# Performance work log

Hardware: AMD Instinct MI355X
Metric: run time of the kernel (lower is better)

The kernel has to match this reference:

```python
import jax, jax.numpy as jnp
import numpy as np

K_NEIGHBORS = 50
MEM_WEIGHT = 0.9  # min(0.9, write_count/10000) saturated
LN_EPS = 1e-5
DIST_EPS = 1e-7


def setup_inputs() -> dict:
    key = jax.random.key(0)
    ks = jax.random.split(key, 10)
    B, S, H, D, M = 4096, 544, 256, 128, 50000
    sc = lambda fan: 1.0 / np.sqrt(fan)
    return {
        "states": jax.random.normal(ks[0], (B, S), jnp.float32),
        "W1": jax.random.normal(ks[1], (S, H), jnp.float32) * sc(S),
        "b1": jnp.zeros((H,), jnp.float32),
        "W2": jax.random.normal(ks[2], (H, D), jnp.float32) * sc(H),
        "b2": jnp.zeros((D,), jnp.float32),
        "ln_g": jnp.ones((D,), jnp.float32),
        "ln_b": jnp.zeros((D,), jnp.float32),
        "mem_keys": jax.random.normal(ks[3], (M, D), jnp.float32),
        "mem_values": jax.random.normal(ks[4], (M,), jnp.float32),
        "V1": jax.random.normal(ks[5], (S, H), jnp.float32) * sc(S),
        "c1": jnp.zeros((H,), jnp.float32),
        "V2": jax.random.normal(ks[6], (H, D), jnp.float32) * sc(H),
        "c2": jnp.zeros((D,), jnp.float32),
        "V3": jax.random.normal(ks[7], (D, 1), jnp.float32) * sc(D),
        "c3": jnp.zeros((1,), jnp.float32),
    }


def _layernorm(x, g, b):
    mu = jnp.mean(x, axis=-1, keepdims=True)
    var = jnp.var(x, axis=-1, keepdims=True)
    return (x - mu) * jax.lax.rsqrt(var + LN_EPS) * g + b


def reference(states, W1, b1, W2, b2, ln_g, ln_b, mem_keys, mem_values,
              V1, c1, V2, c2, V3, c3):
    # --- key encoder: Linear -> ReLU -> Linear -> LayerNorm ---
    h = jax.nn.relu(states @ W1 + b1)            # [B, 256]
    q = _layernorm(h @ W2 + b2, ln_g, ln_b)      # [B, 128]

    # --- DND lookup: squared L2 kNN (FAISS IndexFlatL2 semantics) ---
    # dist2[b, m] = ||q_b - k_m||^2
    q2 = jnp.sum(q * q, axis=-1, keepdims=True)          # [B, 1]
    k2 = jnp.sum(mem_keys * mem_keys, axis=-1)           # [M]
    dist2 = q2 + k2[None, :] - 2.0 * (q @ mem_keys.T)    # [B, M]
    neg_top, idx = jax.lax.top_k(-dist2, K_NEIGHBORS)    # [B, k]
    d = -neg_top                                         # smallest k distances
    w = 1.0 / (d + DIST_EPS)
    w = w / jnp.sum(w, axis=-1, keepdims=True)
    mem_val = jnp.sum(w * mem_values[idx], axis=-1)      # [B]

    # --- value network ---
    v = jax.nn.relu(states @ V1 + c1)
    v = jax.nn.relu(v @ V2 + c2)
    net_val = (v @ V3 + c3)[:, 0]                        # [B]

    return MEM_WEIGHT * mem_val + (1.0 - MEM_WEIGHT) * net_val
```

## Files before the change

kernel.cpp:

```cpp
#include <hip/hip_runtime.h>
#include <stdint.h>

#define B_   4096
#define S_   544
#define H_   256
#define D_   128
#define M_   50000
#define KNN  50
#define NSLICE 8
#define SL_REAL 6250
#define BKEY 64
#define NB   98
#define SL_PAD (NB * BKEY)
#define CAP  128
#define RR   64
#define IMG_U32 5120
#define QT   8

typedef unsigned long long u64;
typedef unsigned int u32;
typedef __attribute__((ext_vector_type(8))) __bf16 bf16x8;
typedef __attribute__((ext_vector_type(8))) unsigned short u16x8;
typedef __attribute__((ext_vector_type(4))) float f32x4;
typedef __attribute__((ext_vector_type(4))) u32 u32x4;

__device__ __forceinline__ u32 bf16_rne(float x) {
  u32 u = __float_as_uint(x);
  return (u + 0x7FFFu + ((u >> 16) & 1u)) >> 16;
}

__device__ __forceinline__ void gl_lds16(const u32* g, u32* l) {
  __builtin_amdgcn_global_load_lds(
      (const __attribute__((address_space(1))) u32*)g,
      (__attribute__((address_space(3))) u32*)l, 16, 0, 0);
}

__global__ __launch_bounds__(256) void k1_gemm(
    const float* __restrict__ A,
    const float* __restrict__ W1, const float* __restrict__ b1,
    const float* __restrict__ V1, const float* __restrict__ c1,
    float* __restrict__ hout, float* __restrict__ v1out)
{
  const float* W    = (blockIdx.z == 0) ? W1 : V1;
  const float* bias = (blockIdx.z == 0) ? b1 : c1;
  float* out        = (blockIdx.z == 0) ? hout : v1out;

  __shared__ float as[16][68];
  __shared__ float bs[16][64];

  int tid = threadIdx.x;
  int tx = tid & 15, ty = tid >> 4;
  int rb = blockIdx.y * 64, cb = blockIdx.x * 64;

  float acc[4][4] = {};

  for (int k0 = 0; k0 < S_; k0 += 16) {
    {
      int r = tid >> 2, k4 = (tid & 3) << 2;
      float4 a = *(const float4*)&A[(size_t)(rb + r) * S_ + k0 + k4];
      as[k4 + 0][r] = a.x; as[k4 + 1][r] = a.y;
      as[k4 + 2][r] = a.z; as[k4 + 3][r] = a.w;
    }
    {
      int kk = tid >> 4, c4 = (tid & 15) << 2;
      *(float4*)&bs[kk][c4] = *(const float4*)&W[(size_t)(k0 + kk) * H_ + cb + c4];
    }
    __syncthreads();
#pragma unroll
    for (int kk = 0; kk < 16; ++kk) {
      float4 a4 = *(const float4*)&as[kk][ty << 2];
      float4 b4 = *(const float4*)&bs[kk][tx << 2];
      float av[4] = {a4.x, a4.y, a4.z, a4.w};
      float bv[4] = {b4.x, b4.y, b4.z, b4.w};
#pragma unroll
      for (int i = 0; i < 4; ++i)
#pragma unroll
        for (int j = 0; j < 4; ++j)
          acc[i][j] = fmaf(av[i], bv[j], acc[i][j]);
    }
    __syncthreads();
  }

#pragma unroll
  for (int i = 0; i < 4; ++i) {
    int r = rb + (ty << 2) + i;
#pragma unroll
    for (int j = 0; j < 4; ++j) {
      int c = cb + (tx << 2) + j;
      float v = acc[i][j] + bias[c];
      out[(size_t)r * H_ + c] = v > 0.0f ? v : 0.0f;
    }
  }
}

__global__ __launch_bounds__(256) void k2_fused(
    const float* __restrict__ A0,
    const float* __restrict__ A1,
    const float* __restrict__ W2, const float* __restrict__ b2,
    const float* __restrict__ V2, const float* __restrict__ c2,
    const float* __restrict__ lng, const float* __restrict__ lnb,
    const float* __restrict__ V3, const float* __restrict__ c3,
    ushort* __restrict__ qext2, float* __restrict__ qrow,
    float* __restrict__ q2out, float* __restrict__ netout)
{
  __shared__ float as[32][36];
  __shared__ float bs[32][132];
  __shared__ float yt[32][132];
  __shared__ float v3s[128];

  int mode = blockIdx.z;
  const float* A    = mode ? A1 : A0;
  const float* W    = mode ? V2 : W2;
  const float* bias = mode ? c2 : b2;

  int tid = threadIdx.x;
  int tx = tid & 31, ty = tid >> 5;
  int rb = blockIdx.x * 32;

  if (mode == 1 && tid < 128) v3s[tid] = V3[tid];

  float acc[4][4] = {};

  for (int k0 = 0; k0 < H_; k0 += 32) {
    {
      int r = tid >> 3, k4 = (tid & 7) << 2;
      float4 a = *(const float4*)&A[(size_t)(rb + r) * H_ + k0 + k4];
      as[k4 + 0][r] = a.x; as[k4 + 1][r] = a.y;
      as[k4 + 2][r] = a.z; as[k4 + 3][r] = a.w;
    }
    {
      int kk = tid >> 3, c16 = (tid & 7) << 4;
#pragma unroll
      for (int t = 0; t < 4; ++t)
        *(float4*)&bs[kk][c16 + (t << 2)] =
            *(const float4*)&W[(size_t)(k0 + kk) * D_ + c16 + (t << 2)];
    }
    __syncthreads();
#pragma unroll
    for (int kk = 0; kk < 32; ++kk) {
      float4 a4 = *(const float4*)&as[kk][ty << 2];
      float4 b4 = *(const float4*)&bs[kk][tx << 2];
      float av[4] = {a4.x, a4.y, a4.z, a4.w};
      float bv[4] = {b4.x, b4.y, b4.z, b4.w};
#pragma unroll
      for (int i = 0; i < 4; ++i)
#pragma unroll
        for (int j = 0; j < 4; ++j)
          acc[i][j] = fmaf(av[i], bv[j], acc[i][j]);
    }
    __syncthreads();
  }

#pragma unroll
  for (int i = 0; i < 4; ++i)
#pragma unroll
    for (int j = 0; j < 4; ++j) {
      int c = (tx << 2) + j;
      yt[(ty << 2) + i][c] = acc[i][j] + bias[c];
    }
  __syncthreads();

  int r8 = tid >> 3, j8 = tid & 7;
  int rg = rb + r8;
  if (mode == 0) {
    float s = 0.f;
#pragma unroll
    for (int t = 0; t < 16; ++t) s += yt[r8][(j8 << 4) + t];
    s += __shfl_xor(s, 1); s += __shfl_xor(s, 2); s += __shfl_xor(s, 4);
    float mu = s * (1.0f / 128.0f);
    float vs = 0.f;
#pragma unroll
    for (int t = 0; t < 16; ++t) {
      float d = yt[r8][(j8 << 4) + t] - mu;
      vs = fmaf(d, d, vs);
    }
    vs += __shfl_xor(vs, 1); vs += __shfl_xor(vs, 2); vs += __shfl_xor(vs, 4);
    float var = vs * (1.0f / 128.0f);
    float rstd = 1.0f / sqrtf(var + 1e-5f);
    float q2p = 0.f;
    ushort* qe = qext2 + (size_t)rg * 128;
#pragma unroll
    for (int t = 0; t < 16; ++t) {
      int c = (j8 << 4) + t;
      float qv = (yt[r8][c] - mu) * rstd * lng[c] + lnb[c];
      qrow[(size_t)rg * D_ + c] = qv;
      qe[c] = (ushort)bf16_rne(-2.0f * qv);
      q2p = fmaf(qv, qv, q2p);
    }
    q2p += __shfl_xor(q2p, 1); q2p += __shfl_xor(q2p, 2); q2p += __shfl_xor(q2p, 4);
    if (j8 == 0) q2out[rg] = q2p;
  } else {
    float s = 0.f;
#pragma unroll
    for (int t = 0; t < 16; ++t) {
      int c = (j8 << 4) + t;
      float v = yt[r8][c];
      v = v > 0.f ? v : 0.f;
      s = fmaf(v, v3s[c], s);
    }
    s += __shfl_xor(s, 1); s += __shfl_xor(s, 2); s += __shfl_xor(s, 4);
    if (j8 == 0) netout[rg] = s + c3[0];
  }
}

__global__ __launch_bounds__(256) void k5_keyimg(
    const float* __restrict__ keys, u32* __restrict__ keyimg,
    float* __restrict__ k2out)
{
  int tid = threadIdx.x;
  int p = blockIdx.x * 128 + (tid >> 1);
  int sub = tid & 1;
  int slice = p / SL_PAD;
  int within = p - slice * SL_PAD;
  int kb = within >> 6, kib = within & 63;
  u32* img = keyimg + (size_t)(slice * NB + kb) * IMG_U32;
  bool real = within < SL_REAL;

  u32 w[32];
  float ss = 0.f;
  if (real) {
    const float* kp = keys + (size_t)(slice * SL_REAL + within) * D_ + sub * 64;
#pragma unroll
    for (int i = 0; i < 16; ++i) {
      float4 x = *(const float4*)(kp + i * 4);
      ss = fmaf(x.x, x.x, fmaf(x.y, x.y, fmaf(x.z, x.z, fmaf(x.w, x.w, ss))));
      w[i * 2]     = bf16_rne(x.x) | (bf16_rne(x.y) << 16);
      w[i * 2 + 1] = bf16_rne(x.z) | (bf16_rne(x.w) << 16);
    }
  } else {
#pragma unroll
    for (int i = 0; i < 32; ++i) w[i] = 0;
  }
#pragma unroll
  for (int cc = 0; cc < 2; ++cc) {
    int c = sub * 2 + cc;
#pragma unroll
    for (int j = 0; j < 4; ++j) {
      u32x4 v = {w[cc*16 + j*4], w[cc*16 + j*4 + 1], w[cc*16 + j*4 + 2], w[cc*16 + j*4 + 3]};
      *(u32x4*)&img[c * 1024 + j * 256 + kib * 4] = v;
    }
  }
  float tot = ss + __shfl_xor(ss, 1);
  if (sub == 0) {
    u32 w0;
    if (real) {
      k2out[slice * SL_REAL + within] = tot;
      u32 h = bf16_rne(tot);
      float hf = __uint_as_float(h << 16);
      u32 lo = bf16_rne(tot - hf);
      w0 = h | (lo << 16);
    } else {
      w0 = 0x7FC07FC0u;
    }
    u32x4 v0 = {w0, 0, 0, 0};
    u32x4 z  = {0, 0, 0, 0};
    *(u32x4*)&img[4 * 1024 + 0 * 256 + kib * 4] = v0;
    *(u32x4*)&img[4 * 1024 + 1 * 256 + kib * 4] = z;
    *(u32x4*)&img[4 * 1024 + 2 * 256 + kib * 4] = z;
    *(u32x4*)&img[4 * 1024 + 3 * 256 + kib * 4] = z;
  }
}

__device__ __forceinline__ void sort128_wave(u32* sb, int lane) {
  for (int k = 2; k <= 128; k <<= 1)
    for (int j = k >> 1; j > 0; j >>= 1) {
#pragma unroll
      for (int half = 0; half < 2; ++half) {
        int e = lane + (half << 6);
        int pp = e ^ j;
        if (pp > e) {
          u32 x = sb[e], y = sb[pp];
          bool up = ((e & k) == 0);
          if ((x > y) == up) { sb[e] = y; sb[pp] = x; }
        }
      }
      __builtin_amdgcn_wave_barrier();
    }
}

#define CSWAP(A, B) do { u32 lo_ = (A) < (B) ? (A) : (B);           \
    u32 hi_ = (A) < (B) ? (B) : (A); (A) = lo_; (B) = hi_; } while (0)

__global__ __launch_bounds__(1024, 8) void k3_knn(
    const ushort* __restrict__ qext2,
    const float* __restrict__ q2g,
    const u32* __restrict__ keyimg,
    u32* __restrict__ lbuf)
{
  __shared__ u32 kbuf[2][IMG_U32];

  int tid = threadIdx.x;
  int l = tid & 63, w = tid >> 6;
  int l15 = l & 15, l4 = l >> 4;
  int wr = w & 3, wc = w >> 2;
  int slice = blockIdx.x & 7;
  int rb = (blockIdx.x >> 3) << 6;

  bf16x8 bfr[4];
#pragma unroll
  for (int c = 0; c < 4; ++c) {
    const ushort* qp = qext2 + (size_t)(rb + wc * 16 + l15) * 128 + c * 32 + l4 * 8;
    bfr[c] = __builtin_bit_cast(bf16x8, *(const u32x4*)qp);
  }
  bf16x8 bk2;
  {
    u16x8 v = {0, 0, 0, 0, 0, 0, 0, 0};
    if (l4 == 0) { v[0] = 0x3F80; v[1] = 0x3F80; }
    bk2 = __builtin_bit_cast(bf16x8, v);
  }
  float q2v = q2g[rb + wc * 16 + l15];

  u32 topq[QT];
#pragma unroll
  for (int j = 0; j < QT; ++j) topq[j] = 0xFFFFFFFFu;

  const u32* imgbase = keyimg + (size_t)slice * NB * IMG_U32;

  auto stage = [&](int b, int t) {
    if (w < 5) {
      const u32* src = imgbase + (size_t)t * IMG_U32 + w * 1024 + l * 4;
      u32* dst = &kbuf[b][w * 1024];
#pragma unroll
      for (int i = 0; i < 4; ++i)
        gl_lds16(src + i * 256, dst + i * 256);
    }
  };

  stage(0, 0);
  __syncthreads();

  int cur = 0;
  for (int t = 0; t < NB; ++t) {
    if (t + 1 < NB) stage(cur ^ 1, t + 1);

    f32x4 acc = {};
#pragma unroll
    for (int c = 0; c < 5; ++c) {
      bf16x8 a = __builtin_bit_cast(bf16x8,
          *(const u32x4*)&kbuf[cur][c * 1024 + l4 * 256 + (wr * 16 + l15) * 4]);
      acc = __builtin_amdgcn_mfma_f32_16x16x32_bf16(a, (c < 4) ? bfr[c] : bk2, acc, 0, 0, 0);
    }

    u32 cc[4];
#pragma unroll
    for (int r = 0; r < 4; ++r) {
      float dd = q2v + acc[r];
      cc[r] = (__float_as_uint(dd) & 0xFFFFE000u) |
              (u32)(t * BKEY + wr * 16 + (l4 << 2) + r);
    }
    CSWAP(cc[0], cc[1]); CSWAP(cc[2], cc[3]);
    CSWAP(cc[0], cc[2]); CSWAP(cc[1], cc[3]);
    CSWAP(cc[1], cc[2]);
    topq[7] = topq[7] < cc[0] ? topq[7] : cc[0];
    topq[6] = topq[6] < cc[1] ? topq[6] : cc[1];
    topq[5] = topq[5] < cc[2] ? topq[5] : cc[2];
    topq[4] = topq[4] < cc[3] ? topq[4] : cc[3];
    CSWAP(topq[0], topq[4]); CSWAP(topq[1], topq[5]);
    CSWAP(topq[2], topq[6]); CSWAP(topq[3], topq[7]);
    CSWAP(topq[0], topq[2]); CSWAP(topq[1], topq[3]);
    CSWAP(topq[4], topq[6]); CSWAP(topq[5], topq[7]);
    CSWAP(topq[0], topq[1]); CSWAP(topq[2], topq[3]);
    CSWAP(topq[4], topq[5]); CSWAP(topq[6], topq[7]);

    __syncthreads();
    cur ^= 1;
  }

  __syncthreads();
  u32* mb = &kbuf[0][0];

#pragma unroll 1
  for (int g = 0; g < 4; ++g) {
    if (wc == g) {
      u32* dst = mb + l15 * 128 + (wr * 4 + l4) * QT;
#pragma unroll
      for (int j = 0; j < QT; ++j) dst[j] = topq[j];
    }
    __syncthreads();

    sort128_wave(mb + w * 128, l);

    if (l < KNN) {
      int grow = rb + g * 16 + w;
      lbuf[((size_t)grow * NSLICE + slice) * CAP + l] = mb[w * 128 + l];
    }
    __syncthreads();
  }
}

__global__ __launch_bounds__(256) void k4_rerank(
    const u32* __restrict__ lbuf, const float* __restrict__ qrow,
    const float* __restrict__ q2g, const float* __restrict__ k2g,
    const float* __restrict__ keys, const float* __restrict__ memv,
    const float* __restrict__ net, float* __restrict__ out)
{
  __shared__ u64 sb[512];
  __shared__ float qs[128];
  __shared__ float part[4][RR];
  __shared__ u64 cand[RR];
  int b = blockIdx.x, t = threadIdx.x;
  if (t < 128) qs[t] = qrow[(size_t)b * D_ + t];
#pragma unroll
  for (int h = 0; h < 2; ++h) {
    int e = t + (h << 8);
    u64 v = ~0ull;
    if (e < NSLICE * KNN) {
      int s = e / KNN, j = e - s * KNN;
      u32 k32 = lbuf[((size_t)b * NSLICE + s) * CAP + j];
      v = ((u64)(k32 & 0xFFFFE000u) << 32) | (u32)(s * SL_REAL + (k32 & 0x1FFFu));
    }
    sb[e] = v;
  }
  __syncthreads();
  for (int k = 2; k <= 512; k <<= 1)
    for (int j = k >> 1; j > 0; j >>= 1) {
#pragma unroll
      for (int h = 0; h < 2; ++h) {
        int e = t + (h << 8);
        int p = e ^ j;
        if (p > e) {
          u64 x = sb[e], y = sb[p];
          bool up = ((e & k) == 0);
          if ((x > y) == up) { sb[e] = y; sb[p] = x; }
        }
      }
      __syncthreads();
    }

  int cid = t & 63, g = t >> 6;
  u32 gidx = (u32)sb[cid];
  const float* kp = keys + (size_t)gidx * D_ + g * 32;
  float dot = 0.f;
#pragma unroll
  for (int i = 0; i < 8; ++i) {
    float4 kv = *(const float4*)(kp + i * 4);
    float4 qv = *(const float4*)&qs[g * 32 + i * 4];
    dot = fmaf(kv.x, qv.x, dot); dot = fmaf(kv.y, qv.y, dot);
    dot = fmaf(kv.z, qv.z, dot); dot = fmaf(kv.w, qv.w, dot);
  }
  part[g][cid] = dot;
  __syncthreads();
  if (t < RR) {
    float dotf = part[0][t] + part[1][t] + part[2][t] + part[3][t];
    u32 gi = (u32)sb[t];
    float dd = q2g[b] + k2g[gi] - 2.0f * dotf;
    cand[t] = ((u64)__float_as_uint(dd) << 32) | gi;
  }
  __syncthreads();
  if (t < 64) {
    for (int k = 2; k <= 64; k <<= 1)
      for (int j = k >> 1; j > 0; j >>= 1) {
        u64 x = cand[t], y = cand[t ^ j];
        __builtin_amdgcn_wave_barrier();
        bool up = ((t & k) == 0);
        u64 mn = x < y ? x : y, mx = x < y ? y : x;
        cand[t] = ((t < (t ^ j)) == up) ? mn : mx;
        __builtin_amdgcn_wave_barrier();
      }
    u64 key = cand[t];
    float d = __uint_as_float((u32)(key >> 32));
    u32 idx = (u32)key;
    float w = 0.f, wv = 0.f;
    if (t < KNN) {
      float ww = 1.0f / (d + 1e-7f);
      w = ww;
      wv = ww * memv[idx];
    }
#pragma unroll
    for (int o = 1; o < 64; o <<= 1) {
      w += __shfl_xor(w, o);
      wv += __shfl_xor(wv, o);
    }
    if (t == 0) out[b] = 0.9f * (wv / w) + 0.1f * net[b];
  }
}

extern "C" void kernel_launch(void* const* d_in, const int* in_sizes, int n_in,
                              void* d_out, int out_size, void* d_ws, size_t ws_size,
                              hipStream_t stream)
{
  const float* states     = (const float*)d_in[0];
  const float* W1         = (const float*)d_in[1];
  const float* b1         = (const float*)d_in[2];
  const float* W2         = (const float*)d_in[3];
  const float* b2         = (const float*)d_in[4];
  const float* lng        = (const float*)d_in[5];
  const float* lnb        = (const float*)d_in[6];
  const float* mem_keys   = (const float*)d_in[7];
  const float* mem_values = (const float*)d_in[8];
  const float* V1         = (const float*)d_in[9];
  const float* c1         = (const float*)d_in[10];
  const float* V2         = (const float*)d_in[11];
  const float* c2         = (const float*)d_in[12];
  const float* V3         = (const float*)d_in[13];
  const float* c3         = (const float*)d_in[14];
  float* out = (float*)d_out;

  char* ws = (char*)d_ws;
  ushort* qext2 = (ushort*)(ws + 0);
  float*  qrow  = (float*)(ws + 1048576);
  float*  q2    = (float*)(ws + 3145728);
  float*  net   = (float*)(ws + 3162112);
  float*  k2g   = (float*)(ws + 3178496);
  u32*  keyimg  = (u32*)(ws + 3383296);
  u32*  lbuf    = (u32*)(ws + 19439616);
  float* h  = (float*)(ws + 3383296);
  float* v1 = (float*)(ws + 3383296 + 4194304);

  k1_gemm<<<dim3(H_ / 64, B_ / 64, 2), 256, 0, stream>>>(states, W1, b1, V1, c1, h, v1);
  k2_fused<<<dim3(B_ / 32, 1, 2), 256, 0, stream>>>(h, v1, W2, b2, V2, c2, lng, lnb, V3, c3,
                                                    qext2, qrow, q2, net);
  k5_keyimg<<<dim3(NSLICE * SL_PAD / 128), 256, 0, stream>>>(mem_keys, keyimg, k2g);
  k3_knn<<<dim3((B_ / 64) * NSLICE), 1024, 0, stream>>>(qext2, q2, keyimg, lbuf);
  k4_rerank<<<dim3(B_), 256, 0, stream>>>(lbuf, qrow, q2, k2g, mem_keys, mem_values, net, out);
}
```

Measured before the change: 259.7 us.

## Fuse key-image build into GEMM launch, deepen kNN staging, merge-based rerank

The first-layer GEMM and the key-image/bf16 conversion kernel now run as one launch, and the h/v1 buffers move so they no longer alias keyimg. The kNN kernel goes from double to quad LDS buffering and processes two tiles per barrier, which halves the number of syncs. The rerank kernel shrinks the candidate stride (CAP 128 to 64) and swaps the full 512-element bitonic sort for a merge of presorted per-slice lists that keeps only the smallest entries. In exchange, kNN uses more LDS per block, which may lower occupancy.

```diff
diff --git a/kernel.cpp b/kernel.cpp
--- a/kernel.cpp
+++ b/kernel.cpp
@@ -12,7 +12,7 @@
 #define BKEY 64
 #define NB   98
 #define SL_PAD (NB * BKEY)
-#define CAP  128
+#define CAP  64
 #define RR   64
 #define IMG_U32 5120
 #define QT   8
@@ -35,61 +35,119 @@
       (__attribute__((address_space(3))) u32*)l, 16, 0, 0);
 }
 
-__global__ __launch_bounds__(256) void k1_gemm(
+__global__ __launch_bounds__(256) void k15_fused(
     const float* __restrict__ A,
     const float* __restrict__ W1, const float* __restrict__ b1,
     const float* __restrict__ V1, const float* __restrict__ c1,
-    float* __restrict__ hout, float* __restrict__ v1out)
+    float* __restrict__ hout, float* __restrict__ v1out,
+    const float* __restrict__ keys, u32* __restrict__ keyimg,
+    float* __restrict__ k2out)
 {
-  const float* W    = (blockIdx.z == 0) ? W1 : V1;
-  const float* bias = (blockIdx.z == 0) ? b1 : c1;
-  float* out        = (blockIdx.z == 0) ? hout : v1out;
-
   __shared__ float as[16][68];
   __shared__ float bs[16][64];
 
   int tid = threadIdx.x;
-  int tx = tid & 15, ty = tid >> 4;
-  int rb = blockIdx.y * 64, cb = blockIdx.x * 64;
-
-  float acc[4][4] = {};
-
-  for (int k0 = 0; k0 < S_; k0 += 16) {
-    {
-      int r = tid >> 2, k4 = (tid & 3) << 2;
-      float4 a = *(const float4*)&A[(size_t)(rb + r) * S_ + k0 + k4];
-      as[k4 + 0][r] = a.x; as[k4 + 1][r] = a.y;
-      as[k4 + 2][r] = a.z; as[k4 + 3][r] = a.w;
-    }
-    {
-      int kk = tid >> 4, c4 = (tid & 15) << 2;
-      *(float4*)&bs[kk][c4] = *(const float4*)&W[(size_t)(k0 + kk) * H_ + cb + c4];
-    }
-    __syncthreads();
-#pragma unroll
-    for (int kk = 0; kk < 16; ++kk) {
-      float4 a4 = *(const float4*)&as[kk][ty << 2];
-      float4 b4 = *(const float4*)&bs[kk][tx << 2];
-      float av[4] = {a4.x, a4.y, a4.z, a4.w};
-      float bv[4] = {b4.x, b4.y, b4.z, b4.w};
-#pragma unroll
-      for (int i = 0; i < 4; ++i)
-#pragma unroll
-        for (int j = 0; j < 4; ++j)
-          acc[i][j] = fmaf(av[i], bv[j], acc[i][j]);
-    }
-    __syncthreads();
-  }
-
-#pragma unroll
-  for (int i = 0; i < 4; ++i) {
-    int r = rb + (ty << 2) + i;
+
+  if (blockIdx.x < 512) {
+    int bx = blockIdx.x;
+    int cb = (bx & 3) * 64, rb = ((bx >> 2) & 63) * 64, zz = bx >> 8;
+    const float* W    = (zz == 0) ? W1 : V1;
+    const float* bias = (zz == 0) ? b1 : c1;
+    float* out        = (zz == 0) ? hout : v1out;
+
+    int tx = tid & 15, ty = tid >> 4;
+    float acc[4][4] = {};
+
+    for (int k0 = 0; k0 < S_; k0 += 16) {
+      {
+        int r = tid >> 2, k4 = (tid & 3) << 2;
+        float4 a = *(const float4*)&A[(size_t)(rb + r) * S_ + k0 + k4];
+        as[k4 + 0][r] = a.x; as[k4 + 1][r] = a.y;
+        as[k4 + 2][r] = a.z; as[k4 + 3][r] = a.w;
+      }
+      {
+        int kk = tid >> 4, c4 = (tid & 15) << 2;
+        *(float4*)&bs[kk][c4] = *(const float4*)&W[(size_t)(k0 + kk) * H_ + cb + c4];
+      }
+      __syncthreads();
+#pragma unroll
+      for (int kk = 0; kk < 16; ++kk) {
+        float4 a4 = *(const float4*)&as[kk][ty << 2];
+        float4 b4 = *(const float4*)&bs[kk][tx << 2];
+        float av[4] = {a4.x, a4.y, a4.z, a4.w};
+        float bv[4] = {b4.x, b4.y, b4.z, b4.w};
+#pragma unroll
+        for (int i = 0; i < 4; ++i)
+#pragma unroll
+          for (int j = 0; j < 4; ++j)
+            acc[i][j] = fmaf(av[i], bv[j], acc[i][j]);
+      }
+      __syncthreads();
+    }
+
+#pragma unroll
+    for (int i = 0; i < 4; ++i) {
+      int r = rb + (ty << 2) + i;
+#pragma unroll
+      for (int j = 0; j < 4; ++j) {
+        int c = cb + (tx << 2) + j;
+        float v = acc[i][j] + bias[c];
+        out[(size_t)r * H_ + c] = v > 0.0f ? v : 0.0f;
+      }
+    }
+    return;
+  }
+
+  int p = (blockIdx.x - 512) * 128 + (tid >> 1);
+  int sub = tid & 1;
+  int slice = p / SL_PAD;
+  int within = p - slice * SL_PAD;
+  int kb = within >> 6, kib = within & 63;
+  u32* img = keyimg + (size_t)(slice * NB + kb) * IMG_U32;
+  bool real = within < SL_REAL;
+
+  u32 w[32];
+  float ss = 0.f;
+  if (real) {
+    const float* kp = keys + (size_t)(slice * SL_REAL + within) * D_ + sub * 64;
+#pragma unroll
+    for (int i = 0; i < 16; ++i) {
+      float4 x = *(const float4*)(kp + i * 4);
+      ss = fmaf(x.x, x.x, fmaf(x.y, x.y, fmaf(x.z, x.z, fmaf(x.w, x.w, ss))));
+      w[i * 2]     = bf16_rne(x.x) | (bf16_rne(x.y) << 16);
+      w[i * 2 + 1] = bf16_rne(x.z) | (bf16_rne(x.w) << 16);
+    }
+  } else {
+#pragma unroll
+    for (int i = 0; i < 32; ++i) w[i] = 0;
+  }
+#pragma unroll
+  for (int cc = 0; cc < 2; ++cc) {
+    int c = sub * 2 + cc;
 #pragma unroll
     for (int j = 0; j < 4; ++j) {
-      int c = cb + (tx << 2) + j;
-      float v = acc[i][j] + bias[c];
-      out[(size_t)r * H_ + c] = v > 0.0f ? v : 0.0f;
-    }
+      u32x4 v = {w[cc*16 + j*4], w[cc*16 + j*4 + 1], w[cc*16 + j*4 + 2], w[cc*16 + j*4 + 3]};
+      *(u32x4*)&img[c * 1024 + j * 256 + kib * 4] = v;
+    }
+  }
+  float tot = ss + __shfl_xor(ss, 1);
+  if (sub == 0) {
+    u32 w0;
+    if (real) {
+      k2out[slice * SL_REAL + within] = tot;
+      u32 h = bf16_rne(tot);
+      float hf = __uint_as_float(h << 16);
+      u32 lo = bf16_rne(tot - hf);
+      w0 = h | (lo << 16);
+    } else {
+      w0 = 0x7FC07FC0u;
+    }
+    u32x4 v0 = {w0, 0, 0, 0};
+    u32x4 z  = {0, 0, 0, 0};
+    *(u32x4*)&img[4 * 1024 + 0 * 256 + kib * 4] = v0;
+    *(u32x4*)&img[4 * 1024 + 1 * 256 + kib * 4] = z;
+    *(u32x4*)&img[4 * 1024 + 2 * 256 + kib * 4] = z;
+    *(u32x4*)&img[4 * 1024 + 3 * 256 + kib * 4] = z;
   }
 }
 
@@ -203,64 +261,6 @@
   }
 }
 
-__global__ __launch_bounds__(256) void k5_keyimg(
-    const float* __restrict__ keys, u32* __restrict__ keyimg,
-    float* __restrict__ k2out)
-{
-  int tid = threadIdx.x;
-  int p = blockIdx.x * 128 + (tid >> 1);
-  int sub = tid & 1;
-  int slice = p / SL_PAD;
-  int within = p - slice * SL_PAD;
-  int kb = within >> 6, kib = within & 63;
-  u32* img = keyimg + (size_t)(slice * NB + kb) * IMG_U32;
-  bool real = within < SL_REAL;
-
-  u32 w[32];
-  float ss = 0.f;
-  if (real) {
-    const float* kp = keys + (size_t)(slice * SL_REAL + within) * D_ + sub * 64;
-#pragma unroll
-    for (int i = 0; i < 16; ++i) {
-      float4 x = *(const float4*)(kp + i * 4);
-      ss = fmaf(x.x, x.x, fmaf(x.y, x.y, fmaf(x.z, x.z, fmaf(x.w, x.w, ss))));
-      w[i * 2]     = bf16_rne(x.x) | (bf16_rne(x.y) << 16);
-      w[i * 2 + 1] = bf16_rne(x.z) | (bf16_rne(x.w) << 16);
-    }
-  } else {
-#pragma unroll
-    for (int i = 0; i < 32; ++i) w[i] = 0;
-  }
-#pragma unroll
-  for (int cc = 0; cc < 2; ++cc) {
-    int c = sub * 2 + cc;
-#pragma unroll
-    for (int j = 0; j < 4; ++j) {
-      u32x4 v = {w[cc*16 + j*4], w[cc*16 + j*4 + 1], w[cc*16 + j*4 + 2], w[cc*16 + j*4 + 3]};
-      *(u32x4*)&img[c * 1024 + j * 256 + kib * 4] = v;
-    }
-  }
-  float tot = ss + __shfl_xor(ss, 1);
-  if (sub == 0) {
-    u32 w0;
-    if (real) {
-      k2out[slice * SL_REAL + within] = tot;
-      u32 h = bf16_rne(tot);
-      float hf = __uint_as_float(h << 16);
-      u32 lo = bf16_rne(tot - hf);
-      w0 = h | (lo << 16);
-    } else {
-      w0 = 0x7FC07FC0u;
-    }
-    u32x4 v0 = {w0, 0, 0, 0};
-    u32x4 z  = {0, 0, 0, 0};
-    *(u32x4*)&img[4 * 1024 + 0 * 256 + kib * 4] = v0;
-    *(u32x4*)&img[4 * 1024 + 1 * 256 + kib * 4] = z;
-    *(u32x4*)&img[4 * 1024 + 2 * 256 + kib * 4] = z;
-    *(u32x4*)&img[4 * 1024 + 3 * 256 + kib * 4] = z;
-  }
-}
-
 __device__ __forceinline__ void sort128_wave(u32* sb, int lane) {
   for (int k = 2; k <= 128; k <<= 1)
     for (int j = k >> 1; j > 0; j >>= 1) {
@@ -287,7 +287,7 @@
     const u32* __restrict__ keyimg,
     u32* __restrict__ lbuf)
 {
-  __shared__ u32 kbuf[2][IMG_U32];
+  __shared__ u32 kbuf[4][IMG_U32];
 
   int tid = threadIdx.x;
   int l = tid & 63, w = tid >> 6;
@@ -326,21 +326,14 @@
     }
   };
 
-  stage(0, 0);
-  __syncthreads();
-
-  int cur = 0;
-  for (int t = 0; t < NB; ++t) {
-    if (t + 1 < NB) stage(cur ^ 1, t + 1);
-
+  auto compute_tile = [&](int t, int bi) {
     f32x4 acc = {};
 #pragma unroll
     for (int c = 0; c < 5; ++c) {
       bf16x8 a = __builtin_bit_cast(bf16x8,
-          *(const u32x4*)&kbuf[cur][c * 1024 + l4 * 256 + (wr * 16 + l15) * 4]);
+          *(const u32x4*)&kbuf[bi][c * 1024 + l4 * 256 + (wr * 16 + l15) * 4]);
       acc = __builtin_amdgcn_mfma_f32_16x16x32_bf16(a, (c < 4) ? bfr[c] : bk2, acc, 0, 0, 0);
     }
-
     u32 cc[4];
 #pragma unroll
     for (int r = 0; r < 4; ++r) {
@@ -361,12 +354,22 @@
     CSWAP(topq[4], topq[6]); CSWAP(topq[5], topq[7]);
     CSWAP(topq[0], topq[1]); CSWAP(topq[2], topq[3]);
     CSWAP(topq[4], topq[5]); CSWAP(topq[6], topq[7]);
-
-    __syncthreads();
-    cur ^= 1;
-  }
-
+  };
+
+  stage(0, 0);
+  stage(1, 1);
   __syncthreads();
+
+#pragma unroll 1
+  for (int k = 0; k < NB / 2; ++k) {
+    int t0 = 2 * k;
+    if (t0 + 2 < NB) stage((t0 + 2) & 3, t0 + 2);
+    if (t0 + 3 < NB) stage((t0 + 3) & 3, t0 + 3);
+    compute_tile(t0, t0 & 3);
+    compute_tile(t0 + 1, (t0 + 1) & 3);
+    __syncthreads();
+  }
+
   u32* mb = &kbuf[0][0];
 
 #pragma unroll 1
@@ -400,32 +403,68 @@
   __shared__ u64 cand[RR];
   int b = blockIdx.x, t = threadIdx.x;
   if (t < 128) qs[t] = qrow[(size_t)b * D_ + t];
+
 #pragma unroll
   for (int h = 0; h < 2; ++h) {
     int e = t + (h << 8);
+    int s = e >> 6, jj = e & 63;
     u64 v = ~0ull;
-    if (e < NSLICE * KNN) {
-      int s = e / KNN, j = e - s * KNN;
-      u32 k32 = lbuf[((size_t)b * NSLICE + s) * CAP + j];
+    if (jj < KNN) {
+      u32 k32 = lbuf[((size_t)b * NSLICE + s) * CAP + jj];
       v = ((u64)(k32 & 0xFFFFE000u) << 32) | (u32)(s * SL_REAL + (k32 & 0x1FFFu));
     }
-    sb[e] = v;
+    int dst = (s & 1) ? ((s << 6) + 63 - jj) : ((s << 6) + jj);
+    sb[dst] = v;
   }
   __syncthreads();
-  for (int k = 2; k <= 512; k <<= 1)
-    for (int j = k >> 1; j > 0; j >>= 1) {
-#pragma unroll
-      for (int h = 0; h < 2; ++h) {
-        int e = t + (h << 8);
-        int p = e ^ j;
-        if (p > e) {
-          u64 x = sb[e], y = sb[p];
-          bool up = ((e & k) == 0);
-          if ((x > y) == up) { sb[e] = y; sb[p] = x; }
-        }
-      }
-      __syncthreads();
-    }
+
+  for (int j = 64; j > 0; j >>= 1) {
+#pragma unroll
+    for (int h = 0; h < 2; ++h) {
+      int g = t + (h << 8);
+      if ((g & j) == 0) {
+        int p = g | j;
+        u64 x = sb[g], y = sb[p];
+        if (y < x) { sb[g] = y; sb[p] = x; }
+      }
+    }
+    __syncthreads();
+  }
+  {
+    int li = t >> 6, jj = t & 63;
+    u64 keep = sb[li * 128 + jj];
+    int dst = (li & 1) ? ((li << 6) + 63 - jj) : ((li << 6) + jj);
+    __syncthreads();
+    sb[dst] = keep;
+    __syncthreads();
+  }
+  for (int j = 64; j > 0; j >>= 1) {
+    if ((t & j) == 0) {
+      int p = t | j;
+      u64 x = sb[t], y = sb[p];
+      if (y < x) { sb[t] = y; sb[p] = x; }
+    }
+    __syncthreads();
+  }
+  {
+    u64 keep = ~0ull; int dst = -1;
+    if (t < 128) {
+      int li = t >> 6, jj = t & 63;
+      keep = sb[li * 128 + jj];
+      dst = li ? (64 + 63 - jj) : jj;
+    }
+    __syncthreads();
+    if (dst >= 0) sb[dst] = keep;
+    __syncthreads();
+  }
+  for (int j = 64; j > 0; j >>= 1) {
+    if (t < 128 && (t & j) == 0) {
+      int p = t | j;
+      u64 x = sb[t], y = sb[p];
+      if (y < x) { sb[t] = y; sb[p] = x; }
+    }
+    __syncthreads();
+  }
 
   int cid = t & 63, g = t >> 6;
   u32 gidx = (u32)sb[cid];
@@ -504,13 +543,13 @@
   float*  k2g   = (float*)(ws + 3178496);
   u32*  keyimg  = (u32*)(ws + 3383296);
   u32*  lbuf    = (u32*)(ws + 19439616);
-  float* h  = (float*)(ws + 3383296);
-  float* v1 = (float*)(ws + 3383296 + 4194304);
-
-  k1_gemm<<<dim3(H_ / 64, B_ / 64, 2), 256, 0, stream>>>(states, W1, b1, V1, c1, h, v1);
+  float* h      = (float*)(ws + 27828224);
+  float* v1     = (float*)(ws + 27828224 + 4194304);
+
+  k15_fused<<<dim3(512 + NSLICE * SL_PAD / 128), 256, 0, stream>>>(
+      states, W1, b1, V1, c1, h, v1, mem_keys, keyimg, k2g);
   k2_fused<<<dim3(B_ / 32, 1, 2), 256, 0, stream>>>(h, v1, W2, b2, V2, c2, lng, lnb, V3, c3,
                                                     qext2, qrow, q2, net);
-  k5_keyimg<<<dim3(NSLICE * SL_PAD / 128), 256, 0, stream>>>(mem_keys, keyimg, k2g);
   k3_knn<<<dim3((B_ / 64) * NSLICE), 1024, 0, stream>>>(qext2, q2, keyimg, lbuf);
   k4_rerank<<<dim3(B_), 256, 0, stream>>>(lbuf, qrow, q2, k2g, mem_keys, mem_values, net, out);
 }
```

Measured after the change: 234.0 us. 1.11x faster.
